# Kernel tuning notes

Measured on AMD Instinct MI355X. Metric: run time of the kernel, lower is better.

The kernel has to match this reference:

```python
import jax, jax.numpy as jnp
import numpy as np

N, L, D = 8, 256, 256  # batch, length, hidden
DP = D + 1             # flag=True appends bias column


def setup_inputs() -> dict:
    key = jax.random.key(0)
    ks = jax.random.split(key, 7)
    s = 0.02  # xavier-like init scale
    return {
        "layer1": jax.random.normal(ks[0], (N, L, D), jnp.float32),
        "layer2": jax.random.normal(ks[1], (N, L, D), jnp.float32),
        "h1": jax.random.normal(ks[2], (N, L, D), jnp.float32),
        "h2": jax.random.normal(ks[3], (N, L, D), jnp.float32),
        "W_1": jax.random.normal(ks[4], (DP, DP, D), jnp.float32) * s,
        "W_2": jax.random.normal(ks[5], (DP, DP, D), jnp.float32) * s,
        "W_3": jax.random.normal(ks[6], (D, D), jnp.float32) * s,
    }


def reference(layer1, layer2, h1, h2, W_1, W_2, W_3):
    n, l, _ = layer1.shape
    ones = jnp.ones((n, l, 1), layer1.dtype)
    l1 = jnp.concatenate([layer1, ones], axis=-1)  # [n, L, D+1]
    l2 = jnp.concatenate([layer2, ones], axis=-1)  # [n, L, D+1]
    # factorized triaffine: two nijc intermediates, then rank contraction
    layer_l = jnp.einsum('nia,abc,njb,nic->nijc', l1, W_1, l2, h1, optimize='optimal')
    layer_r = jnp.einsum('nia,abc,njb,nic->nijc', l1, W_2, l2, h2, optimize='optimal')
    return jnp.einsum('nijc,cd,nijd->nij', layer_l, W_3, layer_r, optimize='optimal')
```

## Files before the change

kernel.cpp:

```cpp
#include <hip/hip_runtime.h>

typedef __attribute__((ext_vector_type(4))) float f32x4;
typedef __attribute__((ext_vector_type(8))) short s16x8;

#define MTOTW 65792

__device__ __forceinline__ short f2bf(float f) {
    unsigned u = __builtin_bit_cast(unsigned, f);
    u = (u + 0x7fffu + ((u >> 16) & 1u)) >> 16;
    return (short)u;
}

__device__ __forceinline__ void gl16(const void* g, void* l) {
    __builtin_amdgcn_global_load_lds(
        (const __attribute__((address_space(1))) unsigned int*)g,
        (__attribute__((address_space(3))) unsigned int*)l, 16, 0, 0);
}


__global__ __launch_bounds__(256) void conv_bf16(
    const float* __restrict__ a, const float* __restrict__ b,
    short* __restrict__ ao, short* __restrict__ bo)
{
    int i = blockIdx.x * 256 + threadIdx.x;
    const int HALF = 131072;
    float4 v; short* dst;
    if (i < HALF) { v = ((const float4*)a)[i]; dst = ao + (size_t)i * 4; }
    else          { v = ((const float4*)b)[i - HALF]; dst = bo + (size_t)(i - HALF) * 4; }
    short4 o; o.x = f2bf(v.x); o.y = f2bf(v.y); o.z = f2bf(v.z); o.w = f2bf(v.w);
    *(short4*)dst = o;
}

__global__ __launch_bounds__(256) void prep_w3t(
    const float* __restrict__ W3, short* __restrict__ W3t)
{
    __shared__ float ld[32][33];
    int t = threadIdx.x, bx = blockIdx.x;
    int c0 = (bx >> 3) * 32, d0 = (bx & 7) * 32;
    int cr = t >> 3, dq = t & 7;
    float4 v = *(const float4*)&W3[(size_t)(c0 + cr) * 256 + d0 + dq * 4];
    ld[cr][dq*4+0] = v.x; ld[cr][dq*4+1] = v.y; ld[cr][dq*4+2] = v.z; ld[cr][dq*4+3] = v.w;
    __syncthreads();
    int dr = t >> 3, cq = t & 7;
    short4 o;
    o.x = f2bf(ld[cq*4+0][dr]); o.y = f2bf(ld[cq*4+1][dr]);
    o.z = f2bf(ld[cq*4+2][dr]); o.w = f2bf(ld[cq*4+3][dr]);
    *(short4*)&W3t[(size_t)(d0 + dr) * 256 + c0 + cq * 4] = o;
}

__global__ __launch_bounds__(256) void prep_wtail(
    const float* __restrict__ W1, const float* __restrict__ W2,
    short* __restrict__ Wtp1, short* __restrict__ Wtp2)
{
    __shared__ float ld[32][33];
    int t = threadIdx.x, bx = blockIdx.x;
    const float* W = blockIdx.y ? W2 : W1;
    short* Wtp = blockIdx.y ? Wtp2 : Wtp1;
    int a0 = (bx >> 3) * 32, c0 = (bx & 7) * 32;
    int ar = t >> 3, cq = t & 7;
    float4 v = *(const float4*)&W[(size_t)(a0 + ar) * MTOTW + 65536 + c0 + cq * 4];
    ld[ar][cq*4+0] = v.x; ld[ar][cq*4+1] = v.y; ld[ar][cq*4+2] = v.z; ld[ar][cq*4+3] = v.w;
    __syncthreads();
    int cr = t >> 3, aq = t & 7;
    short4 o;
    o.x = f2bf(ld[aq*4+0][cr]); o.y = f2bf(ld[aq*4+1][cr]);
    o.z = f2bf(ld[aq*4+2][cr]); o.w = f2bf(ld[aq*4+3][cr]);
    *(short4*)&Wtp[(size_t)(c0 + cr) * 256 + a0 + aq * 4] = o;
}

__global__ __launch_bounds__(256) void prep_wp(
    const float* __restrict__ W1, const float* __restrict__ W2,
    short* __restrict__ Wp1, short* __restrict__ Wp2)
{
    __shared__ float ld[32][33];
    int t = threadIdx.x, bx = blockIdx.x;
    int b = blockIdx.y;
    const float* W = blockIdx.z ? W2 : W1;
    short* Wp = blockIdx.z ? Wp2 : Wp1;
    int a0 = (bx >> 3) * 32, c0 = (bx & 7) * 32;
    int ar = t >> 3, cq = t & 7;
    float4 v = *(const float4*)&W[(size_t)(a0 + ar) * MTOTW + (size_t)b * 256 + c0 + cq * 4];
    ld[ar][cq*4+0] = v.x; ld[ar][cq*4+1] = v.y; ld[ar][cq*4+2] = v.z; ld[ar][cq*4+3] = v.w;
    __syncthreads();
    int cr = t >> 3, aq = t & 7;
    short4 o;
    o.x = f2bf(ld[aq*4+0][cr]); o.y = f2bf(ld[aq*4+1][cr]);
    o.z = f2bf(ld[aq*4+2][cr]); o.w = f2bf(ld[aq*4+3][cr]);
    *(short4*)&Wp[((size_t)(c0 + cr) * 256 + b) * 256 + a0 + aq * 4] = o;
}

__global__ __launch_bounds__(256, 2) void tail_mfma(
    const short* __restrict__ l1b,
    const short* __restrict__ Wtp1, const short* __restrict__ Wtp2,
    const float* __restrict__ W1, const float* __restrict__ W2,
    float* __restrict__ tail1, float* __restrict__ tail2)
{
    __shared__ __align__(16) short Al[128 * 32];
    __shared__ __align__(16) short Bl[128 * 32];
    int t = threadIdx.x, w = t >> 6, lane = t & 63;
    int l4 = lane >> 2, kq = lane & 3;
    int rt = blockIdx.x, nt = blockIdx.y, ten = blockIdx.z;
    const short* Wtp = ten ? Wtp2 : Wtp1;
    const float* Wf = ten ? W2 : W1;
    float* tail = ten ? tail2 : tail1;
    const short* Ab = l1b + (size_t)(rt * 128) * 256;
    const short* Bb = Wtp + (size_t)(nt * 128) * 256;

    f32x4 acc[4][4] = {};
    int m0w = (w >> 1) * 64, n0w = (w & 1) * 64;

    for (int k0 = 0; k0 < 256; k0 += 32) {
        __syncthreads();
        #pragma unroll
        for (int q = 0; q < 4; ++q) {
            int seg = w * 4 + q;
            if (seg < 8)
                gl16(Ab + (size_t)(seg * 16 + l4) * 256 + k0 + kq * 8, &Al[seg * 512]);
            else
                gl16(Bb + (size_t)((seg - 8) * 16 + l4) * 256 + k0 + kq * 8, &Bl[(seg - 8) * 512]);
        }
        __syncthreads();
        s16x8 af[4], bf[4];
        #pragma unroll
        for (int i = 0; i < 4; ++i) {
            af[i] = *(const s16x8*)&Al[(m0w + i * 16 + (lane & 15)) * 32 + (lane >> 4) * 8];
            bf[i] = *(const s16x8*)&Bl[(n0w + i * 16 + (lane & 15)) * 32 + (lane >> 4) * 8];
        }
        #pragma unroll
        for (int mi = 0; mi < 4; ++mi)
            #pragma unroll
            for (int ni = 0; ni < 4; ++ni)
                acc[mi][ni] = __builtin_amdgcn_mfma_f32_16x16x32_bf16(af[mi], bf[ni], acc[mi][ni], 0, 0, 0);
    }
    #pragma unroll
    for (int ni = 0; ni < 4; ++ni) {
        int c = nt * 128 + n0w + ni * 16 + (lane & 15);
        float tl = Wf[(size_t)256 * MTOTW + 65536 + c];
        #pragma unroll
        for (int mi = 0; mi < 4; ++mi) {
            int r = rt * 128 + m0w + mi * 16 + (lane >> 4) * 4;
            #pragma unroll
            for (int reg = 0; reg < 4; ++reg)
                tail[(size_t)(r + reg) * 256 + c] = acc[mi][ni][reg] + tl;
        }
    }
}

__global__ __launch_bounds__(256, 4) void stage1(
    const short* __restrict__ l1b,
    const short* __restrict__ Wp1, const short* __restrict__ Wp2,
    const float* __restrict__ W1, const float* __restrict__ W2,
    short* __restrict__ T1, short* __restrict__ T2, int row0)
{
    __shared__ __align__(16) short S[16384];
    int t = threadIdx.x, w = t >> 6, lane = t & 63;
    int srow8 = lane >> 3;
    int sch   = (lane & 7) ^ srow8;
    int fr    = lane & 15, fb7 = lane & 7;

    unsigned gdx = gridDim.x;
    unsigned orig = blockIdx.x + gdx * (blockIdx.y + 2u * blockIdx.z);
    unsigned nwg = gdx * 1024u;
    unsigned swz = (orig & 7u) * (nwg >> 3) + (orig >> 3);
    unsigned sg  = 2u * gdx;
    unsigned sib = swz % sg;
    unsigned pg  = swz / sg;
    int rt = sib & (gdx - 1u);
    int bt = sib / gdx;
    int zc = pg;

    int c = zc >> 1, ten = zc & 1;
    const short* Wp = ten ? Wp2 : Wp1;
    const float* Wf = ten ? W2 : W1;
    short* T = ten ? T2 : T1;
    int r0g = row0 + rt * 128;
    int b0 = bt * 128;
    const short* Ab = l1b + (size_t)r0g * 256;
    const short* Bb = Wp + ((size_t)c * 256 + b0) * 256;

    f32x4 acc[4][4] = {};
    int m0w = (w >> 1) * 64, n0w = (w & 1) * 64;

    for (int kt = 0; kt < 4; ++kt) {
        int k0 = kt * 64;
        __syncthreads();
        #pragma unroll
        for (int q = 0; q < 8; ++q) {
            int seg = w * 8 + q;
            int rloc = (seg & 15) * 8 + srow8;
            const short* gb = (seg < 16) ? Ab : Bb;
            gl16(gb + (size_t)rloc * 256 + k0 + sch * 8, &S[seg * 512]);
        }
        __syncthreads();
        #pragma unroll
        for (int ss = 0; ss < 2; ++ss) {
            int cx = ((ss * 4 + (lane >> 4)) ^ fb7) * 8;
            s16x8 af[4], bf[4];
            #pragma unroll
            for (int i = 0; i < 4; ++i) {
                af[i] = *(const s16x8*)&S[(m0w + i * 16 + fr) * 64 + cx];
                bf[i] = *(const s16x8*)&S[8192 + (n0w + i * 16 + fr) * 64 + cx];
            }
            #pragma unroll
            for (int mi = 0; mi < 4; ++mi)
                #pragma unroll
                for (int ni = 0; ni < 4; ++ni)
                    acc[mi][ni] = __builtin_amdgcn_mfma_f32_16x16x32_bf16(af[mi], bf[ni], acc[mi][ni], 0, 0, 0);
        }
    }
    __syncthreads();

    short* Cw = &S[w * 4096];
    #pragma unroll
    for (int ni = 0; ni < 4; ++ni) {
        int b = b0 + n0w + ni * 16 + (lane & 15);
        float tl = Wf[(size_t)256 * MTOTW + (size_t)b * 256 + c];
        #pragma unroll
        for (int mi = 0; mi < 4; ++mi)
            #pragma unroll
            for (int reg = 0; reg < 4; ++reg) {
                int lr = mi * 16 + (lane >> 4) * 4 + reg;
                int lc = ni * 16 + (lane & 15);
                Cw[lr * 64 + lc] = f2bf(acc[mi][ni][reg] + tl);
            }
    }
    #pragma unroll
    for (int s = 0; s < 8; ++s) {
        int row = s * 8 + (lane >> 3);
        int co = (lane & 7) * 8;
        int rl = rt * 128 + m0w + row;
        int gb = b0 + n0w + co;
        *(int4*)&T[((size_t)rl * 256 + c) * 256 + gb] = *(int4*)&Cw[row * 64 + co];
    }
}

__global__ __launch_bounds__(256, 2) void stage2(
    const short* __restrict__ l2b,
    const short* __restrict__ T1, const short* __restrict__ T2,
    const float* __restrict__ tail1, const float* __restrict__ tail2,
    const float* __restrict__ h1, const float* __restrict__ h2,
    const short* __restrict__ W3t, float* __restrict__ out, int row0)
{
    __shared__ __align__(16) short S2[36864];
    int t = threadIdx.x, w = t >> 6, lane = t & 63;
    int srow8 = lane >> 3;
    int sch   = (lane & 7) ^ srow8;
    int fr    = lane & 15, fb7 = lane & 7;

    unsigned orig = blockIdx.x + (blockIdx.y << 2);
    unsigned nwg = gridDim.y << 2;
    unsigned swz = (orig & 7u) * (nwg >> 3) + (orig >> 3);
    int jt = swz & 3, rl = swz >> 2;

    int rg = row0 + rl, n = rg >> 8, j0 = jt * 64;
    const short* Arow = l2b + ((size_t)n * 256 + j0) * 256;
    const short* Tt1 = T1 + (size_t)rl * 65536;
    const short* Tt2 = T2 + (size_t)rl * 65536;
    int n0w = w * 64;

    f32x4 acc1[4][4] = {}, acc2[4][4] = {};
    for (int kt = 0; kt < 4; ++kt) {
        int k0 = kt * 64;
        __syncthreads();
        #pragma unroll
        for (int q = 0; q < 18; ++q) {
            int seg = w * 18 + q;
            const short* gb; short* lb; int rloc;
            if (seg < 8)       { rloc = seg * 8 + srow8;        gb = Arow; lb = &S2[seg * 512]; }
            else if (seg < 40) { rloc = (seg - 8) * 8 + srow8;  gb = Tt1;  lb = &S2[4096 + (seg - 8) * 512]; }
            else               { rloc = (seg - 40) * 8 + srow8; gb = Tt2;  lb = &S2[20480 + (seg - 40) * 512]; }
            gl16(gb + (size_t)rloc * 256 + k0 + sch * 8, lb);
        }
        __syncthreads();
        #pragma unroll
        for (int ss = 0; ss < 2; ++ss) {
            int cx = ((ss * 4 + (lane >> 4)) ^ fb7) * 8;
            s16x8 af[4], b1[4], b2[4];
            #pragma unroll
            for (int i = 0; i < 4; ++i) {
                af[i] = *(const s16x8*)&S2[(i * 16 + fr) * 64 + cx];
                b1[i] = *(const s16x8*)&S2[4096 + (n0w + i * 16 + fr) * 64 + cx];
                b2[i] = *(const s16x8*)&S2[20480 + (n0w + i * 16 + fr) * 64 + cx];
            }
            #pragma unroll
            for (int mi = 0; mi < 4; ++mi)
                #pragma unroll
                for (int ni = 0; ni < 4; ++ni) {
                    acc1[mi][ni] = __builtin_amdgcn_mfma_f32_16x16x32_bf16(af[mi], b1[ni], acc1[mi][ni], 0, 0, 0);
                    acc2[mi][ni] = __builtin_amdgcn_mfma_f32_16x16x32_bf16(af[mi], b2[ni], acc2[mi][ni], 0, 0, 0);
                }
        }
    }
    __syncthreads();

    short* V1 = S2;
    f32x4 v2[4][4];
    #pragma unroll
    for (int ni = 0; ni < 4; ++ni) {
        int c = n0w + ni * 16 + (lane & 15);
        float hh1 = h1[(size_t)rg * 256 + c], tl1 = tail1[(size_t)rg * 256 + c];
        float hh2 = h2[(size_t)rg * 256 + c], tl2 = tail2[(size_t)rg * 256 + c];
        #pragma unroll
        for (int mi = 0; mi < 4; ++mi)
            #pragma unroll
            for (int reg = 0; reg < 4; ++reg) {
                int j = mi * 16 + (lane >> 4) * 4 + reg;
                V1[j * 264 + c] = f2bf(hh1 * (acc1[mi][ni][reg] + tl1));
                v2[mi][ni][reg] = hh2 * (acc2[mi][ni][reg] + tl2);
            }
    }
    __syncthreads();

    f32x4 accP[4][4] = {};
    for (int kt = 0; kt < 4; ++kt) {
        int k0 = kt * 64;
        __syncthreads();
        #pragma unroll
        for (int q = 0; q < 8; ++q) {
            int seg = w * 8 + q;
            int rloc = seg * 8 + srow8;
            gl16(W3t + (size_t)rloc * 256 + k0 + sch * 8, &S2[20480 + seg * 512]);
        }
        __syncthreads();
        #pragma unroll
        for (int ss = 0; ss < 2; ++ss) {
            int cx = ((ss * 4 + (lane >> 4)) ^ fb7) * 8;
            s16x8 af[4], bf[4];
            #pragma unroll
            for (int i = 0; i < 4; ++i) {
                af[i] = *(const s16x8*)&V1[(i * 16 + fr) * 264 + k0 + ss * 32 + (lane >> 4) * 8];
                bf[i] = *(const s16x8*)&S2[20480 + (n0w + i * 16 + fr) * 64 + cx];
            }
            #pragma unroll
            for (int mi = 0; mi < 4; ++mi)
                #pragma unroll
                for (int ni = 0; ni < 4; ++ni)
                    accP[mi][ni] = __builtin_amdgcn_mfma_f32_16x16x32_bf16(af[mi], bf[ni], accP[mi][ni], 0, 0, 0);
        }
    }

    float* part = (float*)&S2[16896];
    #pragma unroll
    for (int mi = 0; mi < 4; ++mi)
        #pragma unroll
        for (int reg = 0; reg < 4; ++reg) {
            float s = 0.f;
            #pragma unroll
            for (int ni = 0; ni < 4; ++ni) s += accP[mi][ni][reg] * v2[mi][ni][reg];
            s += __shfl_xor(s, 1); s += __shfl_xor(s, 2);
            s += __shfl_xor(s, 4); s += __shfl_xor(s, 8);
            if ((lane & 15) == 0)
                part[(mi * 16 + (lane >> 4) * 4 + reg) * 4 + w] = s;
        }
    __syncthreads();
    if (t < 64)
        out[(size_t)rg * 256 + j0 + t] = part[t*4] + part[t*4+1] + part[t*4+2] + part[t*4+3];
}

extern "C" void kernel_launch(void* const* d_in, const int* in_sizes, int n_in,
                              void* d_out, int out_size, void* d_ws, size_t ws_size,
                              hipStream_t stream) {
    const float* layer1 = (const float*)d_in[0];
    const float* layer2 = (const float*)d_in[1];
    const float* h1     = (const float*)d_in[2];
    const float* h2     = (const float*)d_in[3];
    const float* W1     = (const float*)d_in[4];
    const float* W2     = (const float*)d_in[5];
    const float* W3     = (const float*)d_in[6];
    float* out = (float*)d_out;

    short* Wp1  = (short*)d_ws;
    short* Wp2  = Wp1 + 16777216;
    short* l1b  = Wp2 + 16777216;
    short* l2b  = l1b + 524288;
    short* W3t  = l2b + 524288;
    short* Wtp1 = W3t + 65536;
    short* Wtp2 = Wtp1 + 65536;
    float* tail1 = (float*)(Wtp2 + 65536);
    float* tail2 = tail1 + 524288;
    short* T1   = (short*)(tail2 + 524288);
    const size_t head = (size_t)(16777216*2 + 524288*2 + 65536*3) * 2 + (size_t)524288 * 2 * 4;
    int chunk = 2048;
    while (head + (size_t)chunk * 262144 > ws_size && chunk > 128) chunk >>= 1;
    short* T2 = T1 + (size_t)chunk * 65536;

    conv_bf16<<<1024, 256, 0, stream>>>(layer1, layer2, l1b, l2b);
    prep_w3t<<<64, 256, 0, stream>>>(W3, W3t);
    prep_wtail<<<dim3(64, 2), 256, 0, stream>>>(W1, W2, Wtp1, Wtp2);
    prep_wp<<<dim3(64, 256, 2), 256, 0, stream>>>(W1, W2, Wp1, Wp2);
    tail_mfma<<<dim3(16, 2, 2), 256, 0, stream>>>(l1b, Wtp1, Wtp2, W1, W2, tail1, tail2);

    for (int row0 = 0; row0 < 2048; row0 += chunk) {
        stage1<<<dim3(chunk / 128, 2, 512), 256, 0, stream>>>(
            l1b, Wp1, Wp2, W1, W2, T1, T2, row0);
        stage2<<<dim3(4, chunk), 256, 0, stream>>>(
            l2b, T1, T2, tail1, tail2, h1, h2, W3t, out, row0);
    }
}
```

Baseline: 680.1 us.

## Double-buffer stage2 GEMM loads and split into two sequential half phases

```diff
diff --git a/kernel.cpp b/kernel.cpp
--- a/kernel.cpp
+++ b/kernel.cpp
@@ -241,7 +241,7 @@
     const float* __restrict__ h1, const float* __restrict__ h2,
     const short* __restrict__ W3t, float* __restrict__ out, int row0)
 {
-    __shared__ __align__(16) short S2[36864];
+    __shared__ __align__(16) short S2[40960];
     int t = threadIdx.x, w = t >> 6, lane = t & 63;
     int srow8 = lane >> 3;
     int sch   = (lane & 7) ^ srow8;
@@ -259,41 +259,60 @@
     int n0w = w * 64;
 
     f32x4 acc1[4][4] = {}, acc2[4][4] = {};
-    for (int kt = 0; kt < 4; ++kt) {
-        int k0 = kt * 64;
-        __syncthreads();
-        #pragma unroll
-        for (int q = 0; q < 18; ++q) {
-            int seg = w * 18 + q;
-            const short* gb; short* lb; int rloc;
-            if (seg < 8)       { rloc = seg * 8 + srow8;        gb = Arow; lb = &S2[seg * 512]; }
-            else if (seg < 40) { rloc = (seg - 8) * 8 + srow8;  gb = Tt1;  lb = &S2[4096 + (seg - 8) * 512]; }
-            else               { rloc = (seg - 40) * 8 + srow8; gb = Tt2;  lb = &S2[20480 + (seg - 40) * 512]; }
-            gl16(gb + (size_t)rloc * 256 + k0 + sch * 8, lb);
-        }
-        __syncthreads();
-        #pragma unroll
-        for (int ss = 0; ss < 2; ++ss) {
-            int cx = ((ss * 4 + (lane >> 4)) ^ fb7) * 8;
-            s16x8 af[4], b1[4], b2[4];
-            #pragma unroll
-            for (int i = 0; i < 4; ++i) {
-                af[i] = *(const s16x8*)&S2[(i * 16 + fr) * 64 + cx];
-                b1[i] = *(const s16x8*)&S2[4096 + (n0w + i * 16 + fr) * 64 + cx];
-                b2[i] = *(const s16x8*)&S2[20480 + (n0w + i * 16 + fr) * 64 + cx];
-            }
-            #pragma unroll
-            for (int mi = 0; mi < 4; ++mi)
+
+    auto half_phase = [&](const short* Tt, f32x4 (&acc)[4][4]) {
+        #pragma unroll
+        for (int q = 0; q < 10; ++q) {
+            int seg = w * 10 + q;
+            if (seg < 8) gl16(Arow + (size_t)(seg * 8 + srow8) * 256 + sch * 8, &S2[seg * 512]);
+            else         gl16(Tt + (size_t)((seg - 8) * 8 + srow8) * 256 + sch * 8, &S2[4096 + (seg - 8) * 512]);
+        }
+        __builtin_amdgcn_sched_barrier(0);
+        for (int kt = 0; kt < 4; ++kt) {
+            int cur = (kt & 1) * 20480;
+            if (kt < 3) {
+                int nb = 20480 - cur, k0 = (kt + 1) * 64;
                 #pragma unroll
-                for (int ni = 0; ni < 4; ++ni) {
-                    acc1[mi][ni] = __builtin_amdgcn_mfma_f32_16x16x32_bf16(af[mi], b1[ni], acc1[mi][ni], 0, 0, 0);
-                    acc2[mi][ni] = __builtin_amdgcn_mfma_f32_16x16x32_bf16(af[mi], b2[ni], acc2[mi][ni], 0, 0, 0);
+                for (int q = 0; q < 10; ++q) {
+                    int seg = w * 10 + q;
+                    if (seg < 8) gl16(Arow + (size_t)(seg * 8 + srow8) * 256 + k0 + sch * 8, &S2[nb + seg * 512]);
+                    else         gl16(Tt + (size_t)((seg - 8) * 8 + srow8) * 256 + k0 + sch * 8, &S2[nb + 4096 + (seg - 8) * 512]);
                 }
-        }
-    }
+                __builtin_amdgcn_sched_barrier(0);
+                asm volatile("s_waitcnt vmcnt(10)" ::: "memory");
+            } else {
+                asm volatile("s_waitcnt vmcnt(0)" ::: "memory");
+            }
+            __builtin_amdgcn_s_barrier();
+            __builtin_amdgcn_sched_barrier(0);
+            #pragma unroll
+            for (int ss = 0; ss < 2; ++ss) {
+                int cx = ((ss * 4 + (lane >> 4)) ^ fb7) * 8;
+                s16x8 af[4], bf[4];
+                #pragma unroll
+                for (int i = 0; i < 4; ++i) {
+                    af[i] = *(const s16x8*)&S2[cur + (i * 16 + fr) * 64 + cx];
+                    bf[i] = *(const s16x8*)&S2[cur + 4096 + (n0w + i * 16 + fr) * 64 + cx];
+                }
+                #pragma unroll
+                for (int mi = 0; mi < 4; ++mi)
+                    #pragma unroll
+                    for (int ni = 0; ni < 4; ++ni)
+                        acc[mi][ni] = __builtin_amdgcn_mfma_f32_16x16x32_bf16(af[mi], bf[ni], acc[mi][ni], 0, 0, 0);
+            }
+            __builtin_amdgcn_sched_barrier(0);
+            __builtin_amdgcn_s_barrier();
+            __builtin_amdgcn_sched_barrier(0);
+        }
+    };
+    half_phase(Tt1, acc1);
+    half_phase(Tt2, acc2);
+
     __syncthreads();
 
     short* V1 = S2;
+    float* part = (float*)&S2[16896];
+
     f32x4 v2[4][4];
     #pragma unroll
     for (int ni = 0; ni < 4; ++ni) {
@@ -309,7 +328,6 @@
                 v2[mi][ni][reg] = hh2 * (acc2[mi][ni][reg] + tl2);
             }
     }
-    __syncthreads();
 
     f32x4 accP[4][4] = {};
     for (int kt = 0; kt < 4; ++kt) {
@@ -319,7 +337,7 @@
         for (int q = 0; q < 8; ++q) {
             int seg = w * 8 + q;
             int rloc = seg * 8 + srow8;
-            gl16(W3t + (size_t)rloc * 256 + k0 + sch * 8, &S2[20480 + seg * 512]);
+            gl16(W3t + (size_t)rloc * 256 + k0 + sch * 8, &S2[17408 + seg * 512]);
         }
         __syncthreads();
         #pragma unroll
@@ -329,7 +347,7 @@
             #pragma unroll
             for (int i = 0; i < 4; ++i) {
                 af[i] = *(const s16x8*)&V1[(i * 16 + fr) * 264 + k0 + ss * 32 + (lane >> 4) * 8];
-                bf[i] = *(const s16x8*)&S2[20480 + (n0w + i * 16 + fr) * 64 + cx];
+                bf[i] = *(const s16x8*)&S2[17408 + (n0w + i * 16 + fr) * 64 + cx];
             }
             #pragma unroll
             for (int mi = 0; mi < 4; ++mi)
@@ -339,7 +357,6 @@
         }
     }
 
-    float* part = (float*)&S2[16896];
     #pragma unroll
     for (int mi = 0; mi < 4; ++mi)
         #pragma unroll
```

Measured after the change: 644.1 us. -5.3%, faster.
